# Optimization experiments

Hardware: AMD Instinct MI355X
Metric: run time of the kernel (lower is better)

Reference implementation:

```python
import jax, jax.numpy as jnp
import numpy as np

DIM = 2048
N_HEADS = 16
Q_RANK = 1536
KV_RANK = 512
D_NOPE = 128
D_ROPE = 64
D_V = 128
EPS = 1e-6
B, S = 2, 2048
ROPE_THETA = 10000.0


def rmsnorm(x, w, eps=EPS):
    return x * jax.lax.rsqrt(jnp.mean(x * x, axis=-1, keepdims=True) + eps) * w


def apply_rope(x):
    # x: [b, h, s, d] with d even; LLaMA-style interleaved pair rotation
    b, h, s, d = x.shape
    inv_freq = 1.0 / (ROPE_THETA ** (jnp.arange(0, d, 2, dtype=jnp.float32) / d))
    ang = jnp.arange(s, dtype=jnp.float32)[:, None] * inv_freq[None, :]  # [s, d/2]
    cos, sin = jnp.cos(ang), jnp.sin(ang)
    xr = x.reshape(b, h, s, d // 2, 2)
    x1, x2 = xr[..., 0], xr[..., 1]
    o1 = x1 * cos - x2 * sin
    o2 = x1 * sin + x2 * cos
    return jnp.stack([o1, o2], axis=-1).reshape(b, h, s, d)


def setup_inputs() -> dict:
    key = jax.random.key(0)
    ks = jax.random.split(key, 10)
    std = 0.02
    return {
        "x": jax.random.normal(ks[0], (B, S, DIM), dtype=jnp.float32),
        "wq_down": jax.random.normal(ks[1], (Q_RANK, DIM), dtype=jnp.float32) * std,
        "q_norm_w": jnp.ones((Q_RANK,), dtype=jnp.float32),
        "wq_up": jax.random.normal(ks[2], (N_HEADS * D_NOPE, Q_RANK), dtype=jnp.float32) * std,
        "wq_rope": jax.random.normal(ks[3], (N_HEADS * D_ROPE, Q_RANK), dtype=jnp.float32) * std,
        "wkv_down": jax.random.normal(ks[4], (KV_RANK, DIM), dtype=jnp.float32) * std,
        "kv_norm_w": jnp.ones((KV_RANK,), dtype=jnp.float32),
        "wkv_up": jax.random.normal(ks[5], (N_HEADS * (D_NOPE + D_V), KV_RANK), dtype=jnp.float32) * std,
        "wk_rope": jax.random.normal(ks[6], (D_ROPE, DIM), dtype=jnp.float32) * std,
        "wo": jax.random.normal(ks[7], (DIM, N_HEADS * D_V), dtype=jnp.float32) * std,
    }


def reference(x, wq_down, q_norm_w, wq_up, wq_rope, wkv_down, kv_norm_w, wkv_up, wk_rope, wo):
    bs, s, _ = x.shape
    # low-rank Q path
    q_c = rmsnorm(x @ wq_down.T, q_norm_w)                              # [b,s,qr]
    q_nope = (q_c @ wq_up.T).reshape(bs, s, N_HEADS, D_NOPE).transpose(0, 2, 1, 3)
    q_pe = (q_c @ wq_rope.T).reshape(bs, s, N_HEADS, D_ROPE).transpose(0, 2, 1, 3)
    # low-rank KV path
    kv_c = rmsnorm(x @ wkv_down.T, kv_norm_w)                           # [b,s,kvr]
    kv_up = (kv_c @ wkv_up.T).reshape(bs, s, N_HEADS, D_NOPE + D_V)
    k_nope = kv_up[..., :D_NOPE].transpose(0, 2, 1, 3)                  # [b,h,s,dn]
    v = kv_up[..., D_NOPE:].transpose(0, 2, 1, 3)                       # [b,h,s,dv]
    # shared rope key (1 head), broadcast across heads
    k_rope = (x @ wk_rope.T).reshape(bs, s, 1, D_ROPE).transpose(0, 2, 1, 3)  # [b,1,s,dr]
    q_pe = apply_rope(q_pe)
    k_rope = apply_rope(k_rope)
    q = jnp.concatenate([q_nope, q_pe], axis=-1)                        # [b,h,s,dn+dr]
    k = jnp.concatenate([k_nope, jnp.broadcast_to(k_rope, (bs, N_HEADS, s, D_ROPE))], axis=-1)
    scale = 1.0 / np.sqrt(D_NOPE + D_ROPE)
    scores = jnp.einsum('bhqd,bhkd->bhqk', q, k) * scale                # [b,h,s,s]
    causal = jnp.tril(jnp.ones((s, s), dtype=bool))
    scores = jnp.where(causal, scores, -jnp.inf)
    probs = jax.nn.softmax(scores, axis=-1)
    out = jnp.einsum('bhqk,bhkv->bhqv', probs, v)                       # [b,h,s,dv]
    out = out.transpose(0, 2, 1, 3).reshape(bs, s, N_HEADS * D_V)
    return out @ wo.T
```

## Files before the change

### kernel.cpp

```cpp
#include <hip/hip_runtime.h>
#include <stdint.h>

typedef _Float16 f16x8 __attribute__((ext_vector_type(8)));
typedef _Float16 f16x4 __attribute__((ext_vector_type(4)));
typedef float fx4 __attribute__((ext_vector_type(4)));

static constexpr int S_LEN = 2048;
static constexpr int BATCH = 2;
static constexpr int TOKENS = BATCH * S_LEN;
static constexpr int DIM = 2048;
static constexpr int NH = 16;
static constexpr int QR = 1536;
static constexpr int KVR = 512;
static constexpr int DN = 128;
static constexpr int DR = 64;
static constexpr int DV = 128;

__device__ __forceinline__ void async16(const _Float16* g, _Float16* lds_base_uniform) {
  __builtin_amdgcn_global_load_lds(
      (const __attribute__((address_space(1))) void*)g,
      (__attribute__((address_space(3))) void*)lds_base_uniform, 16, 0, 0);
}

__device__ __forceinline__ void bar() {
  asm volatile("" ::: "memory");
  __builtin_amdgcn_s_barrier();
  asm volatile("" ::: "memory");
}
#define VMWAIT(n) asm volatile("s_waitcnt vmcnt(" #n ")" ::: "memory")

#define ROR16(x, ctrl) \
  __uint_as_float(__builtin_amdgcn_update_dpp(__float_as_uint(x), __float_as_uint(x), \
                                              (ctrl), 0xF, 0xF, false))

__device__ __forceinline__ void sincos_rev(float ang, float* sn, float* cs) {
  float rev = ang * 0.15915494309189535f;
  rev -= floorf(rev);
  *sn = __builtin_amdgcn_sinf(rev);
  *cs = __builtin_amdgcn_cosf(rev);
}

struct CvtSegs {
  const float* src[8];
  _Float16* dst[8];
  const float* nw[8];
  int nmod[8];
  int n4[8];
  int cum[9];
};
__global__ __launch_bounds__(256) void cvt_all(CvtSegs s) {
  const int b = blockIdx.x;
  int seg = 0;
#pragma unroll
  for (int k = 0; k < 7; ++k) seg += (b >= s.cum[seg + 1]) ? 1 : 0;
  const int i = (b - s.cum[seg]) * 256 + threadIdx.x;
  if (i >= s.n4[seg]) return;
  fx4 v = *(const fx4*)(s.src[seg] + (size_t)i * 4);
  if (s.nw[seg]) {
    const int c0 = (int)(((size_t)i * 4) % (size_t)s.nmod[seg]);
    fx4 wv = *(const fx4*)(s.nw[seg] + c0);
    v[0] *= wv[0]; v[1] *= wv[1]; v[2] *= wv[2]; v[3] *= wv[3];
  }
  f16x4 o;
  o[0] = (_Float16)v[0]; o[1] = (_Float16)v[1];
  o[2] = (_Float16)v[2]; o[3] = (_Float16)v[3];
  *(f16x4*)(s.dst[seg] + (size_t)i * 4) = o;
}

__global__ __launch_bounds__(256) void rownorm(const _Float16* __restrict__ qc,
                                               const _Float16* __restrict__ kvc,
                                               float* __restrict__ rq,
                                               float* __restrict__ rkv) {
  const int idx = blockIdx.x * 4 + (threadIdx.x >> 6);
  const int lane = threadIdx.x & 63;
  const bool isq = idx < TOKENS;
  const int row = isq ? idx : idx - TOKENS;
  const int NC = isq ? QR : KVR;
  const f16x8* p = (const f16x8*)((isq ? qc : kvc) + (size_t)row * NC);
  float ss = 0.f;
  for (int c = lane; c < NC / 8; c += 64) {
    f16x8 v = p[c];
#pragma unroll
    for (int e = 0; e < 8; ++e) { const float x = (float)v[e]; ss += x * x; }
  }
#pragma unroll
  for (int d = 1; d < 64; d <<= 1) ss += __shfl_xor(ss, d);
  if (lane == 0) {
    const float rv = rsqrtf(ss / (float)NC + 1e-6f);
    if (isq) rq[row] = rv; else rkv[row] = rv;
  }
}

template <int MODE>
__global__ __launch_bounds__(256) void gemm_nt(const _Float16* __restrict__ A,
                                               const _Float16* __restrict__ W,
                                               void* __restrict__ C0v,
                                               void* __restrict__ C1v,
                                               void* __restrict__ C2v,
                                               int M, int N, int K) {
  __shared__ __attribute__((aligned(16))) _Float16 As[3][128 * 32];
  __shared__ __attribute__((aligned(16))) _Float16 Ws[3][128 * 32];
  const int tid = threadIdx.x;
  const int lane = tid & 63;
  const int wave = tid >> 6;
  const int wr = (wave >> 1) * 64;
  const int wc = (wave & 1) * 64;
  const int m16 = lane & 15;
  const int quad = lane >> 4;
  const int swz = (m16 >> 1) & 3;
  const int m0 = blockIdx.y * 128;
  const int n0 = blockIdx.x * 128;

  auto stage = [&](int buf, int k0) {
#pragma unroll
    for (int p = 0; p < 2; ++p) {
      const int cb = p * 256 + wave * 64;
      const int ch = cb + lane;
      const int r = ch >> 2;
      const int c8 = ((ch & 3) ^ ((r >> 1) & 3)) * 8;
      async16(A + (size_t)(m0 + r) * K + k0 + c8, &As[buf][cb * 8]);
      async16(W + (size_t)(n0 + r) * K + k0 + c8, &Ws[buf][cb * 8]);
    }
  };

  const fx4 fz = {0.f, 0.f, 0.f, 0.f};
  fx4 acc[4][4];
#pragma unroll
  for (int i = 0; i < 4; ++i)
#pragma unroll
    for (int j = 0; j < 4; ++j) acc[i][j] = fz;

  const int nkt = K >> 5;
  stage(0, 0);
  stage(1, 32);
  int cur = 0;
  for (int kt = 0; kt < nkt; ++kt) {
    if (kt + 1 < nkt) { VMWAIT(4); } else { VMWAIT(0); }
    bar();
    if (kt + 2 < nkt) {
      int b2 = cur + 2; if (b2 >= 3) b2 -= 3;
      stage(b2, (kt + 2) * 32);
    }
    const _Float16* as = As[cur];
    const _Float16* ws = Ws[cur];
    f16x8 af[4], wf[4];
#pragma unroll
    for (int i = 0; i < 4; ++i)
      af[i] = *(const f16x8*)(&as[((wr + i * 16 + m16) * 4 + (quad ^ swz)) * 8]);
#pragma unroll
    for (int j = 0; j < 4; ++j)
      wf[j] = *(const f16x8*)(&ws[((wc + j * 16 + m16) * 4 + (quad ^ swz)) * 8]);
#pragma unroll
    for (int i = 0; i < 4; ++i)
#pragma unroll
      for (int j = 0; j < 4; ++j)
        acc[i][j] = __builtin_amdgcn_mfma_f32_16x16x32_f16(af[i], wf[j], acc[i][j], 0, 0, 0);
    if (++cur == 3) cur = 0;
  }

#pragma unroll
  for (int j = 0; j < 4; ++j) {
    const int col = n0 + wc + j * 16 + m16;
    if (MODE == 5) {
      if (col < 2048) {
#pragma unroll
        for (int i = 0; i < 4; ++i)
#pragma unroll
          for (int r = 0; r < 4; ++r) {
            const size_t row = (size_t)(m0 + wr + i * 16 + quad * 4 + r);
            const _Float16 v = (_Float16)acc[i][j][r];
            if (col < 1536) ((_Float16*)C0v)[row * 1536 + col] = v;
            else            ((_Float16*)C1v)[row * 512 + col - 1536] = v;
          }
      } else if (col < 2112) {
        const int d = col - 2048;
        const int pidx = d >> 1;
        const bool odd = (d & 1);
        const float fr = exp2f(-(float)pidx * 0.4152410118609203f);
#pragma unroll
        for (int i = 0; i < 4; ++i)
#pragma unroll
          for (int r = 0; r < 4; ++r) {
            const size_t row = (size_t)(m0 + wr + i * 16 + quad * 4 + r);
            const int spos = (int)(row & (S_LEN - 1));
            float sn, cs;
            sincos_rev((float)spos * fr, &sn, &cs);
            const float own = acc[i][j][r];
            const float oth = __shfl_xor(own, 1);
            const float res = odd ? (oth * sn + own * cs) : (own * cs - oth * sn);
            ((_Float16*)C2v)[row * 64 + d] = (_Float16)res;
          }
      }
    } else {
      if (col < N) {
#pragma unroll
        for (int i = 0; i < 4; ++i)
#pragma unroll
          for (int r = 0; r < 4; ++r) {
            const size_t row = (size_t)(m0 + wr + i * 16 + quad * 4 + r);
            ((float*)C0v)[row * N + col] = acc[i][j][r];
          }
      }
    }
  }
}

__global__ __launch_bounds__(256) void gemm_up(
    const _Float16* __restrict__ qc, const _Float16* __restrict__ wqu,
    const _Float16* __restrict__ kvc, const _Float16* __restrict__ wkvu,
    const float* __restrict__ rq, const float* __restrict__ rkv,
    _Float16* __restrict__ qnope, _Float16* __restrict__ qpe,
    _Float16* __restrict__ knope, _Float16* __restrict__ vT) {
  __shared__ __attribute__((aligned(16))) _Float16 As[3][128 * 32];
  __shared__ __attribute__((aligned(16))) _Float16 Ws[3][128 * 32];
  const int tid = threadIdx.x;
  const int lane = tid & 63;
  const int wave = tid >> 6;
  const int wr = (wave >> 1) * 64;
  const int wc = (wave & 1) * 64;
  const int m16 = lane & 15;
  const int quad = lane >> 4;
  const int swz = (m16 >> 1) & 3;
  const int m0 = blockIdx.y * 128;
  const bool isq = (blockIdx.x < 24);
  const int n0 = (isq ? blockIdx.x : blockIdx.x - 24) * 128;
  const _Float16* A = isq ? qc : kvc;
  const _Float16* W = isq ? wqu : wkvu;
  const int K = isq ? QR : KVR;

  auto stage = [&](int buf, int k0) {
#pragma unroll
    for (int p = 0; p < 2; ++p) {
      const int cb = p * 256 + wave * 64;
      const int ch = cb + lane;
      const int r = ch >> 2;
      const int c8 = ((ch & 3) ^ ((r >> 1) & 3)) * 8;
      async16(A + (size_t)(m0 + r) * K + k0 + c8, &As[buf][cb * 8]);
      async16(W + (size_t)(n0 + r) * K + k0 + c8, &Ws[buf][cb * 8]);
    }
  };

  const fx4 fz = {0.f, 0.f, 0.f, 0.f};
  fx4 acc[4][4];
#pragma unroll
  for (int i = 0; i < 4; ++i)
#pragma unroll
    for (int j = 0; j < 4; ++j) acc[i][j] = fz;

  const int nkt = K >> 5;
  stage(0, 0);
  stage(1, 32);
  int cur = 0;
  for (int kt = 0; kt < nkt; ++kt) {
    if (kt + 1 < nkt) { VMWAIT(4); } else { VMWAIT(0); }
    bar();
    if (kt + 2 < nkt) {
      int b2 = cur + 2; if (b2 >= 3) b2 -= 3;
      stage(b2, (kt + 2) * 32);
    }
    const _Float16* as = As[cur];
    const _Float16* ws = Ws[cur];
    f16x8 af[4], wf[4];
#pragma unroll
    for (int i = 0; i < 4; ++i)
      af[i] = *(const f16x8*)(&as[((wr + i * 16 + m16) * 4 + (quad ^ swz)) * 8]);
#pragma unroll
    for (int j = 0; j < 4; ++j)
      wf[j] = *(const f16x8*)(&ws[((wc + j * 16 + m16) * 4 + (quad ^ swz)) * 8]);
#pragma unroll
    for (int i = 0; i < 4; ++i)
#pragma unroll
      for (int j = 0; j < 4; ++j)
        acc[i][j] = __builtin_amdgcn_mfma_f32_16x16x32_f16(af[i], wf[j], acc[i][j], 0, 0, 0);
    if (++cur == 3) cur = 0;
  }

  const float* rs = isq ? rq : rkv;
  float rsq[4][4];
#pragma unroll
  for (int i = 0; i < 4; ++i)
#pragma unroll
    for (int r = 0; r < 4; ++r)
      rsq[i][r] = rs[m0 + wr + i * 16 + quad * 4 + r];

#pragma unroll
  for (int j = 0; j < 4; ++j) {
    const int col = n0 + wc + j * 16 + m16;
    if (isq) {
#pragma unroll
      for (int i = 0; i < 4; ++i)
#pragma unroll
        for (int r = 0; r < 4; ++r) {
          const size_t row = (size_t)(m0 + wr + i * 16 + quad * 4 + r);
          const _Float16 v = (_Float16)(acc[i][j][r] * rsq[i][r]);
          if (col < 2048) qnope[row * 2048 + col] = v;
          else qpe[row * 1024 + col - 2048] = v;
        }
    } else {
      const int head = col >> 8;
      const int sub = col & 255;
      if (sub < 128) {
#pragma unroll
        for (int i = 0; i < 4; ++i)
#pragma unroll
          for (int r = 0; r < 4; ++r)
            knope[(size_t)(m0 + wr + i * 16 + quad * 4 + r) * 2048 + head * 128 + sub] =
                (_Float16)(acc[i][j][r] * rsq[i][r]);
      } else {
        const int dv = sub - 128;
#pragma unroll
        for (int i = 0; i < 4; ++i) {
          f16x4 v;
#pragma unroll
          for (int r = 0; r < 4; ++r) v[r] = (_Float16)(acc[i][j][r] * rsq[i][r]);
          *(f16x4*)(&vT[(size_t)(head * 128 + dv) * TOKENS + m0 + wr + i * 16 + quad * 4]) = v;
        }
      }
    }
  }
}

__global__ __launch_bounds__(512, 4) void mla_attn(
    const _Float16* __restrict__ qn,
    const _Float16* __restrict__ qp,
    const _Float16* __restrict__ kn,
    const _Float16* __restrict__ kr,
    const _Float16* __restrict__ vT,
    _Float16* __restrict__ out)
{
  __shared__ __attribute__((aligned(16))) _Float16 Ks[2][768 * 8];
  __shared__ __attribute__((aligned(16))) _Float16 Vs[2][512 * 8];
  __shared__ __attribute__((aligned(16))) _Float16 Ps[8][16][40];

  const int bid = blockIdx.x;
  const int j = bid >> 5;
  const int bh = bid & 31;
  const int b = bh >> 4;
  const int h = bh & 15;
  const int q16 = 15 - j;
  const int qb = q16 * 128;
  const int tok0 = b * S_LEN;

  const int tid = threadIdx.x;
  const int lane = tid & 63;
  const int wave = tid >> 6;
  const int m16 = lane & 15;
  const int quad = lane >> 4;
  const int R0 = qb + wave * 16;

  auto stageKV = [&](int buf, int kbase) {
#pragma unroll
    for (int jj = 0; jj < 3; ++jj) {
      const int idx = wave * 3 + jj;
      if (idx < 12) {
        const int ch = idx * 2 + (lane >> 5);
        const int key = lane & 31;
        const _Float16* g = (ch < 16)
            ? kn + (size_t)(tok0 + kbase + key) * 2048 + h * 128 + ch * 8
            : kr + (size_t)(tok0 + kbase + key) * 64 + (ch - 16) * 8;
        async16(g, &Ks[buf][idx * 512]);
      } else if (idx < 20) {
        const int iv = idx - 12;
        const int p = iv * 64 + lane;
        const int L = p ^ ((p >> 3) & 3);
        const int dv = L >> 2;
        const int qcc = L & 3;
        async16(vT + (size_t)(h * 128 + dv) * TOKENS + tok0 + kbase + qcc * 8,
                &Vs[buf][iv * 512]);
      }
    }
  };

  const float scale2 = 0.07216878364870323f * 1.4426950408889634f;
  const fx4 fz = {0.f, 0.f, 0.f, 0.f};

  f16x8 qf[6];
  {
    const int srow = qb + wave * 16 + m16;
    const size_t t = (size_t)(tok0 + srow);
#pragma unroll
    for (int kk = 0; kk < 4; ++kk)
      qf[kk] = *(const f16x8*)(qn + t * 2048 + h * 128 + kk * 32 + quad * 8);
#pragma unroll
    for (int kk = 0; kk < 2; ++kk) {
      f16x8 v = *(const f16x8*)(qp + t * 1024 + h * 64 + kk * 32 + quad * 8);
      f16x8 o;
      const int i0 = kk * 16 + quad * 4;
#pragma unroll
      for (int jj = 0; jj < 4; ++jj) {
        const float ang = (float)srow * exp2f(-(float)(i0 + jj) * 0.4152410118609203f);
        float sn, cs;
        sincos_rev(ang, &sn, &cs);
        const float x1 = (float)v[2 * jj], x2 = (float)v[2 * jj + 1];
        o[2 * jj]     = (_Float16)(x1 * cs - x2 * sn);
        o[2 * jj + 1] = (_Float16)(x1 * sn + x2 * cs);
      }
      qf[4 + kk] = o;
    }
  }

  fx4 oacc[9];
#pragma unroll
  for (int n = 0; n < 9; ++n) oacc[n] = fz;
  float mst[4];
#pragma unroll
  for (int r = 0; r < 4; ++r) mst[r] = -3.0e38f;
  f16x8 vones;
#pragma unroll
  for (int e = 0; e < 8; ++e) vones[e] = (_Float16)1.0f;

  const int nkt = (qb >> 5) + 4;

  stageKV(0, 0);
  for (int kt = 0; kt < nkt; ++kt) {
    const int kbase = kt * 32;
    __syncthreads();
    if (kt + 1 < nkt) stageKV((kt + 1) & 1, kbase + 32);

    const bool live = (kbase <= R0 + 15);
    if (!live) continue;
    const _Float16* ks = Ks[kt & 1];
    const _Float16* vs = Vs[kt & 1];

    fx4 sc[2];
    sc[0] = fz; sc[1] = fz;
    __builtin_amdgcn_s_setprio(1);
#pragma unroll
    for (int kk = 0; kk < 6; ++kk) {
#pragma unroll
      for (int n = 0; n < 2; ++n) {
        f16x8 kf = *(const f16x8*)(&ks[(kk * 128 + quad * 32 + n * 16 + m16) * 8]);
        sc[n] = __builtin_amdgcn_mfma_f32_16x16x32_f16(qf[kk], kf, sc[n], 0, 0, 0);
      }
    }
    __builtin_amdgcn_s_setprio(0);

    f16x8 vf[8];
#pragma unroll
    for (int n8 = 0; n8 < 8; ++n8) {
      const int c0 = (n8 * 16 + m16) * 4 + quad;
      vf[n8] = *(const f16x8*)(&vs[(c0 ^ ((c0 >> 3) & 3)) * 8]);
    }

    const bool needmask = (kbase + 31 > R0);
    float alpha[4];
    bool any_upd = false;
#pragma unroll
    for (int r = 0; r < 4; ++r) {
      float v0 = sc[0][r] * scale2;
      float v1 = sc[1][r] * scale2;
      if (needmask) {
        const int qrow = R0 + quad * 4 + r;
        if (kbase + m16 > qrow)      v0 = -3.0e38f;
        if (kbase + 16 + m16 > qrow) v1 = -3.0e38f;
      }
      const float pre = fmaxf(v0, v1);
      float al = 1.0f;
      if (__any(pre > mst[r] + 10.0f)) {
        float mx = pre;
        mx = fmaxf(mx, ROR16(mx, 0x128));
        mx = fmaxf(mx, ROR16(mx, 0x124));
        mx = fmaxf(mx, ROR16(mx, 0x122));
        mx = fmaxf(mx, ROR16(mx, 0x121));
        const float mn = fmaxf(mst[r], mx);
        al = exp2f(mst[r] - mn);
        mst[r] = mn;
        any_upd = true;
      }
      alpha[r] = al;
      const float p0 = exp2f(v0 - mst[r]);
      const float p1 = exp2f(v1 - mst[r]);
      _Float16* pr = &Ps[wave][quad * 4 + r][0];
      pr[m16] = (_Float16)p0;
      pr[16 + m16] = (_Float16)p1;
    }
    if (any_upd) {
#pragma unroll
      for (int n8 = 0; n8 < 9; ++n8)
#pragma unroll
        for (int r = 0; r < 4; ++r) oacc[n8][r] *= alpha[r];
    }

    f16x8 pf = *(const f16x8*)(&Ps[wave][m16][quad * 8]);
    __builtin_amdgcn_s_setprio(1);
#pragma unroll
    for (int n8 = 0; n8 < 8; ++n8)
      oacc[n8] = __builtin_amdgcn_mfma_f32_16x16x32_f16(pf, vf[n8], oacc[n8], 0, 0, 0);
    oacc[8] = __builtin_amdgcn_mfma_f32_16x16x32_f16(pf, vones, oacc[8], 0, 0, 0);
    __builtin_amdgcn_s_setprio(0);
  }

  float inv[4];
#pragma unroll
  for (int r = 0; r < 4; ++r) inv[r] = 1.0f / oacc[8][r];
#pragma unroll
  for (int n8 = 0; n8 < 8; ++n8) {
#pragma unroll
    for (int r = 0; r < 4; ++r) {
      const size_t t = (size_t)(tok0 + qb + wave * 16 + quad * 4 + r);
      out[t * 2048 + h * 128 + n8 * 16 + m16] = (_Float16)(oacc[n8][r] * inv[r]);
    }
  }
}

extern "C" void kernel_launch(void* const* d_in, const int* in_sizes, int n_in,
                              void* d_out, int out_size, void* d_ws, size_t ws_size,
                              hipStream_t stream) {
  const float* x         = (const float*)d_in[0];
  const float* wq_down   = (const float*)d_in[1];
  const float* q_norm_w  = (const float*)d_in[2];
  const float* wq_up     = (const float*)d_in[3];
  const float* wq_rope   = (const float*)d_in[4];
  const float* wkv_down  = (const float*)d_in[5];
  const float* kv_norm_w = (const float*)d_in[6];
  const float* wkv_up    = (const float*)d_in[7];
  const float* wk_rope   = (const float*)d_in[8];
  const float* wo        = (const float*)d_in[9];
  float* out = (float*)d_out;

  char* ws = (char*)d_ws;
  size_t off = 0;
  auto alloc = [&](size_t bytes) {
    char* p = ws + off;
    off += (bytes + 255) & ~(size_t)255;
    return p;
  };
  _Float16* x_h     = (_Float16*)alloc((size_t)TOKENS * DIM * 2);
  _Float16* wA_h    = (_Float16*)alloc((size_t)2176 * DIM * 2);
  _Float16* wquqr_h = (_Float16*)alloc((size_t)3072 * QR * 2);
  _Float16* wkvu_h  = (_Float16*)alloc((size_t)NH * 256 * KVR * 2);
  _Float16* wo_h    = (_Float16*)alloc((size_t)DIM * NH * DV * 2);
  _Float16* qc_h    = (_Float16*)alloc((size_t)TOKENS * QR * 2);
  _Float16* kvc_h   = (_Float16*)alloc((size_t)TOKENS * KVR * 2);
  _Float16* qnope_h = (_Float16*)alloc((size_t)TOKENS * 2048 * 2);
  _Float16* qpe_h   = (_Float16*)alloc((size_t)TOKENS * 1024 * 2);
  _Float16* knope_h = (_Float16*)alloc((size_t)TOKENS * 2048 * 2);
  _Float16* vT_h    = (_Float16*)alloc((size_t)2048 * TOKENS * 2);
  _Float16* krope_h = (_Float16*)alloc((size_t)TOKENS * DR * 2);
  _Float16* attn_h  = (_Float16*)alloc((size_t)TOKENS * 2048 * 2);
  float* rq_h       = (float*)alloc((size_t)TOKENS * 4);
  float* rkv_h      = (float*)alloc((size_t)TOKENS * 4);

  CvtSegs cs;
  const float* srcs[8] = {x, wq_down, wq_up, wq_rope, wkv_down, wk_rope, wkv_up, wo};
  _Float16* dsts[8] = {x_h, wA_h, wquqr_h, wquqr_h + (size_t)2048 * QR,
                       wA_h + (size_t)1536 * DIM, wA_h + (size_t)2048 * DIM,
                       wkvu_h, wo_h};
  const float* nws[8] = {nullptr, nullptr, q_norm_w, q_norm_w, nullptr, nullptr,
                         kv_norm_w, nullptr};
  const int nmods[8] = {4, 4, QR, QR, 4, 4, KVR, 4};
  const size_t ns[8] = {(size_t)TOKENS * DIM, (size_t)QR * DIM, (size_t)2048 * QR,
                        (size_t)1024 * QR, (size_t)KVR * DIM, (size_t)DR * DIM,
                        (size_t)NH * 256 * KVR, (size_t)DIM * NH * DV};
  int cum = 0;
  for (int i = 0; i < 8; ++i) {
    cs.src[i] = srcs[i];
    cs.dst[i] = dsts[i];
    cs.nw[i] = nws[i];
    cs.nmod[i] = nmods[i];
    cs.n4[i] = (int)(ns[i] / 4);
    cs.cum[i] = cum;
    cum += (cs.n4[i] + 255) / 256;
  }
  cs.cum[8] = cum;
  cvt_all<<<dim3(cum), 256, 0, stream>>>(cs);

  const unsigned gm = TOKENS / 128;

  gemm_nt<5><<<dim3(17, gm), 256, 0, stream>>>(x_h, wA_h, qc_h, kvc_h, krope_h,
                                               TOKENS, 2112, DIM);
  rownorm<<<dim3(2 * TOKENS / 4), 256, 0, stream>>>(qc_h, kvc_h, rq_h, rkv_h);
  gemm_up<<<dim3(24 + 32, gm), 256, 0, stream>>>(qc_h, wquqr_h, kvc_h, wkvu_h,
                                                 rq_h, rkv_h,
                                                 qnope_h, qpe_h, knope_h, vT_h);
  mla_attn<<<dim3(512), 512, 0, stream>>>(qnope_h, qpe_h, knope_h, krope_h, vT_h, attn_h);
  gemm_nt<1><<<dim3(16, gm), 256, 0, stream>>>(attn_h, wo_h, out, nullptr, nullptr,
                                               TOKENS, DIM, NH * DV);
}
```

Before: 544.6 us.

## Replace up-projection and output GEMMs with 256x256 tiled 8-wave kernel

Introduces a templated gemm256 kernel that uses 256x256 output tiles, 512 threads and a K-step of 64. Loads are double-buffered in quarter stages interleaved with four MFMA quadrants, with XOR-swizzled LDS and s_setprio around the MFMA bursts. It replaces both the fused Q/KV up-projection and the output projection, aiming for more data reuse per tile loaded and better overlap of loads with math. In exchange the grids get much smaller (28x16 and 8x16 blocks), which may underfill the GPU's CUs, and LDS and register pressure rise. The attention kernel's launch bounds are also relaxed from 4 to 2 blocks per CU.

New measurement: 452.6 us. -16.9%, faster.

```diff
diff --git a/kernel.cpp b/kernel.cpp
--- a/kernel.cpp
+++ b/kernel.cpp
@@ -205,122 +205,186 @@
   }
 }
 
-__global__ __launch_bounds__(256) void gemm_up(
-    const _Float16* __restrict__ qc, const _Float16* __restrict__ wqu,
-    const _Float16* __restrict__ kvc, const _Float16* __restrict__ wkvu,
+template <int MODE>
+__global__ __launch_bounds__(512, 2) void gemm256(
+    const _Float16* __restrict__ Aq, const _Float16* __restrict__ Wq,
+    const _Float16* __restrict__ Akv, const _Float16* __restrict__ Wkv,
     const float* __restrict__ rq, const float* __restrict__ rkv,
-    _Float16* __restrict__ qnope, _Float16* __restrict__ qpe,
-    _Float16* __restrict__ knope, _Float16* __restrict__ vT) {
-  __shared__ __attribute__((aligned(16))) _Float16 As[3][128 * 32];
-  __shared__ __attribute__((aligned(16))) _Float16 Ws[3][128 * 32];
+    void* __restrict__ C0, void* __restrict__ C1,
+    void* __restrict__ C2, void* __restrict__ C3, int Kq) {
+  __shared__ __attribute__((aligned(16))) _Float16 As[2][256 * 64];
+  __shared__ __attribute__((aligned(16))) _Float16 Ws[2][256 * 64];
+
   const int tid = threadIdx.x;
   const int lane = tid & 63;
   const int wave = tid >> 6;
-  const int wr = (wave >> 1) * 64;
-  const int wc = (wave & 1) * 64;
+  const int wrow = wave >> 2;
+  const int wcol = wave & 3;
   const int m16 = lane & 15;
   const int quad = lane >> 4;
-  const int swz = (m16 >> 1) & 3;
-  const int m0 = blockIdx.y * 128;
-  const bool isq = (blockIdx.x < 24);
-  const int n0 = (isq ? blockIdx.x : blockIdx.x - 24) * 128;
-  const _Float16* A = isq ? qc : kvc;
-  const _Float16* W = isq ? wqu : wkvu;
-  const int K = isq ? QR : KVR;
-
-  auto stage = [&](int buf, int k0) {
-#pragma unroll
-    for (int p = 0; p < 2; ++p) {
-      const int cb = p * 256 + wave * 64;
+  const int m0 = blockIdx.y * 256;
+
+  const bool isq = (MODE == 0) || ((int)blockIdx.x < 12);
+  const int n0 = (MODE == 0) ? blockIdx.x * 256
+                             : (isq ? blockIdx.x * 256 : (blockIdx.x - 12) * 256);
+  const _Float16* A = (MODE == 0) ? Aq : (isq ? Aq : Akv);
+  const _Float16* W = (MODE == 0) ? Wq : (isq ? Wq : Wkv);
+  const int K = (MODE == 0) ? Kq : (isq ? QR : KVR);
+
+  auto stageHalf = [&](int buf, int k0, int tensor, int h) {
+#pragma unroll
+    for (int k = 0; k < 2; ++k) {
+      const int cb = (wave * 2 + k) * 64;
       const int ch = cb + lane;
-      const int r = ch >> 2;
-      const int c8 = ((ch & 3) ^ ((r >> 1) & 3)) * 8;
-      async16(A + (size_t)(m0 + r) * K + k0 + c8, &As[buf][cb * 8]);
-      async16(W + (size_t)(n0 + r) * K + k0 + c8, &Ws[buf][cb * 8]);
+      const int r = ch >> 3;
+      const int gc = (ch & 7) ^ (r & 7);
+      const int grow = h * 128 + r;
+      if (tensor == 0)
+        async16(A + (size_t)(m0 + grow) * K + k0 + gc * 8,
+                &As[buf][(h * 1024 + cb) * 8]);
+      else
+        async16(W + (size_t)(n0 + grow) * K + k0 + gc * 8,
+                &Ws[buf][(h * 1024 + cb) * 8]);
     }
   };
 
   const fx4 fz = {0.f, 0.f, 0.f, 0.f};
-  fx4 acc[4][4];
-#pragma unroll
-  for (int i = 0; i < 4; ++i)
+  fx4 acc[8][4];
+#pragma unroll
+  for (int i = 0; i < 8; ++i)
 #pragma unroll
     for (int j = 0; j < 4; ++j) acc[i][j] = fz;
 
-  const int nkt = K >> 5;
-  stage(0, 0);
-  stage(1, 32);
-  int cur = 0;
-  for (int kt = 0; kt < nkt; ++kt) {
-    if (kt + 1 < nkt) { VMWAIT(4); } else { VMWAIT(0); }
-    bar();
-    if (kt + 2 < nkt) {
-      int b2 = cur + 2; if (b2 >= 3) b2 -= 3;
-      stage(b2, (kt + 2) * 32);
-    }
+  f16x8 af[4][2], wf0[2][2], wf1[2][2];
+
+  auto rdA = [&](const _Float16* as, int mh) {
+#pragma unroll
+    for (int mg = 0; mg < 4; ++mg)
+#pragma unroll
+      for (int ks = 0; ks < 2; ++ks) {
+        const int row = mh * 128 + mg * 32 + wrow * 16 + m16;
+        af[mg][ks] = *(const f16x8*)(&as[(row * 8 + ((ks * 4 + quad) ^ (m16 & 7))) * 8]);
+      }
+  };
+  auto rdB = [&](const _Float16* ws, int nh, f16x8 wf[2][2]) {
+#pragma unroll
+    for (int ng = 0; ng < 2; ++ng)
+#pragma unroll
+      for (int ks = 0; ks < 2; ++ks) {
+        const int row = nh * 128 + ng * 64 + wcol * 16 + m16;
+        wf[ng][ks] = *(const f16x8*)(&ws[(row * 8 + ((ks * 4 + quad) ^ (m16 & 7))) * 8]);
+      }
+  };
+  auto quadMFMA = [&](int mh, int nh, f16x8 wf[2][2]) {
+    __builtin_amdgcn_s_setprio(1);
+#pragma unroll
+    for (int ks = 0; ks < 2; ++ks)
+#pragma unroll
+      for (int mg = 0; mg < 4; ++mg)
+#pragma unroll
+        for (int ng = 0; ng < 2; ++ng)
+          acc[mh * 4 + mg][nh * 2 + ng] = __builtin_amdgcn_mfma_f32_16x16x32_f16(
+              af[mg][ks], wf[ng][ks], acc[mh * 4 + mg][nh * 2 + ng], 0, 0, 0);
+    __builtin_amdgcn_s_setprio(0);
+  };
+
+  const int nkt = K >> 6;
+  stageHalf(0, 0, 0, 0);
+  stageHalf(0, 0, 1, 0);
+  stageHalf(0, 0, 1, 1);
+  stageHalf(0, 0, 0, 1);
+
+  for (int t = 0; t < nkt; ++t) {
+    const int cur = t & 1;
+    const int nb = cur ^ 1;
+    const int k0n = (t + 1) * 64;
+    const bool more = (t + 1 < nkt);
     const _Float16* as = As[cur];
     const _Float16* ws = Ws[cur];
-    f16x8 af[4], wf[4];
-#pragma unroll
-    for (int i = 0; i < 4; ++i)
-      af[i] = *(const f16x8*)(&as[((wr + i * 16 + m16) * 4 + (quad ^ swz)) * 8]);
-#pragma unroll
-    for (int j = 0; j < 4; ++j)
-      wf[j] = *(const f16x8*)(&ws[((wc + j * 16 + m16) * 4 + (quad ^ swz)) * 8]);
-#pragma unroll
-    for (int i = 0; i < 4; ++i)
-#pragma unroll
-      for (int j = 0; j < 4; ++j)
-        acc[i][j] = __builtin_amdgcn_mfma_f32_16x16x32_f16(af[i], wf[j], acc[i][j], 0, 0, 0);
-    if (++cur == 3) cur = 0;
-  }
-
-  const float* rs = isq ? rq : rkv;
-  float rsq[4][4];
-#pragma unroll
-  for (int i = 0; i < 4; ++i)
-#pragma unroll
-    for (int r = 0; r < 4; ++r)
-      rsq[i][r] = rs[m0 + wr + i * 16 + quad * 4 + r];
-
-#pragma unroll
-  for (int j = 0; j < 4; ++j) {
-    const int col = n0 + wc + j * 16 + m16;
-    if (isq) {
-#pragma unroll
-      for (int i = 0; i < 4; ++i)
+
+    VMWAIT(4);
+    bar();
+    rdA(as, 0);
+    rdB(ws, 0, wf0);
+    if (more) stageHalf(nb, k0n, 0, 0);
+    quadMFMA(0, 0, wf0);
+
+    if (more) { VMWAIT(4); } else { VMWAIT(2); }
+    bar();
+    rdB(ws, 1, wf1);
+    if (more) stageHalf(nb, k0n, 1, 0);
+    quadMFMA(0, 1, wf1);
+
+    if (more) { VMWAIT(4); } else { VMWAIT(0); }
+    bar();
+    rdA(as, 1);
+    if (more) stageHalf(nb, k0n, 1, 1);
+    quadMFMA(1, 1, wf1);
+
+    bar();
+    if (more) stageHalf(nb, k0n, 0, 1);
+    quadMFMA(1, 0, wf0);
+  }
+
+  float rsq[8][4];
+  if (MODE == 1) {
+    const float* rs = isq ? rq : rkv;
+#pragma unroll
+    for (int mg = 0; mg < 8; ++mg)
+#pragma unroll
+      for (int r = 0; r < 4; ++r)
+        rsq[mg][r] = rs[m0 + mg * 32 + wrow * 16 + quad * 4 + r];
+  }
+
+#pragma unroll
+  for (int ng = 0; ng < 4; ++ng) {
+    const int col = n0 + ng * 64 + wcol * 16 + m16;
+    if (MODE == 0) {
+#pragma unroll
+      for (int mg = 0; mg < 8; ++mg)
 #pragma unroll
         for (int r = 0; r < 4; ++r) {
-          const size_t row = (size_t)(m0 + wr + i * 16 + quad * 4 + r);
-          const _Float16 v = (_Float16)(acc[i][j][r] * rsq[i][r]);
-          if (col < 2048) qnope[row * 2048 + col] = v;
-          else qpe[row * 1024 + col - 2048] = v;
+          const size_t row = (size_t)(m0 + mg * 32 + wrow * 16 + quad * 4 + r);
+          ((float*)C0)[row * 2048 + col] = acc[mg][ng][r];
+        }
+    } else if (isq) {
+#pragma unroll
+      for (int mg = 0; mg < 8; ++mg)
+#pragma unroll
+        for (int r = 0; r < 4; ++r) {
+          const size_t row = (size_t)(m0 + mg * 32 + wrow * 16 + quad * 4 + r);
+          const _Float16 v = (_Float16)(acc[mg][ng][r] * rsq[mg][r]);
+          if (col < 2048) ((_Float16*)C0)[row * 2048 + col] = v;
+          else ((_Float16*)C1)[row * 1024 + col - 2048] = v;
         }
     } else {
       const int head = col >> 8;
       const int sub = col & 255;
       if (sub < 128) {
 #pragma unroll
-        for (int i = 0; i < 4; ++i)
-#pragma unroll
-          for (int r = 0; r < 4; ++r)
-            knope[(size_t)(m0 + wr + i * 16 + quad * 4 + r) * 2048 + head * 128 + sub] =
-                (_Float16)(acc[i][j][r] * rsq[i][r]);
+        for (int mg = 0; mg < 8; ++mg)
+#pragma unroll
+          for (int r = 0; r < 4; ++r) {
+            const size_t row = (size_t)(m0 + mg * 32 + wrow * 16 + quad * 4 + r);
+            ((_Float16*)C2)[row * 2048 + head * 128 + sub] =
+                (_Float16)(acc[mg][ng][r] * rsq[mg][r]);
+          }
       } else {
         const int dv = sub - 128;
 #pragma unroll
-        for (int i = 0; i < 4; ++i) {
+        for (int mg = 0; mg < 8; ++mg) {
           f16x4 v;
 #pragma unroll
-          for (int r = 0; r < 4; ++r) v[r] = (_Float16)(acc[i][j][r] * rsq[i][r]);
-          *(f16x4*)(&vT[(size_t)(head * 128 + dv) * TOKENS + m0 + wr + i * 16 + quad * 4]) = v;
+          for (int r = 0; r < 4; ++r) v[r] = (_Float16)(acc[mg][ng][r] * rsq[mg][r]);
+          *(f16x4*)(&((_Float16*)C3)[(size_t)(head * 128 + dv) * TOKENS + m0 +
+                                     mg * 32 + wrow * 16 + quad * 4]) = v;
         }
       }
     }
   }
 }
 
-__global__ __launch_bounds__(512, 4) void mla_attn(
+__global__ __launch_bounds__(512, 2) void mla_attn(
     const _Float16* __restrict__ qn,
     const _Float16* __restrict__ qp,
     const _Float16* __restrict__ kn,
@@ -570,10 +634,11 @@
   gemm_nt<5><<<dim3(17, gm), 256, 0, stream>>>(x_h, wA_h, qc_h, kvc_h, krope_h,
                                                TOKENS, 2112, DIM);
   rownorm<<<dim3(2 * TOKENS / 4), 256, 0, stream>>>(qc_h, kvc_h, rq_h, rkv_h);
-  gemm_up<<<dim3(24 + 32, gm), 256, 0, stream>>>(qc_h, wquqr_h, kvc_h, wkvu_h,
-                                                 rq_h, rkv_h,
-                                                 qnope_h, qpe_h, knope_h, vT_h);
+  gemm256<1><<<dim3(12 + 16, TOKENS / 256), 512, 0, stream>>>(
+      qc_h, wquqr_h, kvc_h, wkvu_h, rq_h, rkv_h,
+      qnope_h, qpe_h, knope_h, vT_h, 0);
   mla_attn<<<dim3(512), 512, 0, stream>>>(qnope_h, qpe_h, knope_h, krope_h, vT_h, attn_h);
-  gemm_nt<1><<<dim3(16, gm), 256, 0, stream>>>(attn_h, wo_h, out, nullptr, nullptr,
-                                               TOKENS, DIM, NH * DV);
-}
+  gemm256<0><<<dim3(8, TOKENS / 256), 512, 0, stream>>>(
+      attn_h, wo_h, nullptr, nullptr, nullptr, nullptr,
+      out, nullptr, nullptr, nullptr, NH * DV);
+}
```
